# Kernel optimization log

Measured on AMD Instinct MI355X. Metric: run time of the kernel, lower is better.

The kernel has to match this reference:

```python
import jax, jax.numpy as jnp
import numpy as np

MULTI_INFER_NUM = 8
D_EMBED = 128
T, B = 512, 32


def setup_inputs() -> dict:
    key = jax.random.key(0)
    k1, k2, k3 = jax.random.split(key, 3)
    positions = jax.random.randint(k1, (T, B), 0, 16, dtype=jnp.int64)
    outputs = jax.random.normal(k2, (T, B, D_EMBED), dtype=jnp.float32)
    table = jax.random.normal(k3, (MULTI_INFER_NUM + 1, D_EMBED, D_EMBED), dtype=jnp.float32)
    return {"positions": positions, "outputs": outputs, "table": table}


def reference(positions, outputs, table):
    # clip positions >= multi_infer_num to the sentinel row multi_infer_num
    r_positions = jnp.where(positions < MULTI_INFER_NUM, positions, MULTI_INFER_NUM)
    # gather per-(t,b) d x d transfer matrices: [T, B, d, d]
    positions_embedding = table[r_positions]
    # batched matvec: [T, B, d]
    transferred = jnp.einsum('ibde,ibd->ibe', positions_embedding, outputs)
    return transferred
```

## Files before the change

kernel.cpp:

```cpp
#include <hip/hip_runtime.h>
#include <hip/hip_bf16.h>

#define TBPAIRS 16384
#define DEMB    128
#define NRROWS  9
#define BP      64

using short8 = __attribute__((ext_vector_type(8))) short;
using f32x4  = __attribute__((ext_vector_type(4))) float;

__device__ __forceinline__ unsigned short f2bf(float f) {
    unsigned u = __float_as_uint(f);
    u = u + 0x7FFFu + ((u >> 16) & 1u);
    return (unsigned short)(u >> 16);
}

__global__ __launch_bounds__(256) void pack_table_kernel(
    const float* __restrict__ table, uint4* __restrict__ bpack) {
    const int r = blockIdx.x;
    const float* M = table + r * DEMB * DEMB;
    for (int idx = threadIdx.x; idx < 2048; idx += 256) {
        const int lane = idx & 63;
        const int ks   = (idx >> 6) & 3;
        const int nt   = idx >> 8;
        const int e    = nt * 16 + (lane & 15);
        const int d0   = ks * 32 + (lane >> 4) * 8;
        union { unsigned short us[8]; uint4 v; } u;
#pragma unroll
        for (int j = 0; j < 8; ++j)
            u.us[j] = f2bf(M[(d0 + j) * DEMB + e]);
        bpack[r * 2048 + idx] = u.v;
    }
}

__global__ __launch_bounds__(256) void transfer_kernel(
    const int*   __restrict__ positions,
    const float* __restrict__ x,
    const uint4* __restrict__ bpack,
    float*       __restrict__ out) {

    __shared__ unsigned char list[NRROWS][BP];
    __shared__ int cnt[NRROWS];
    __shared__ unsigned char tile_r[16];
    __shared__ unsigned char tile_s[16];
    __shared__ int ntiles;

    const int tid   = threadIdx.x;
    const int pair0 = blockIdx.x * BP;

    if (tid < NRROWS) cnt[tid] = 0;
    __syncthreads();

    if (tid < BP) {
        int p = positions[pair0 + tid];
        int r = (p < 8) ? p : 8;
        int rank = atomicAdd(&cnt[r], 1);
        list[r][rank] = (unsigned char)tid;
    }
    __syncthreads();

    if (tid == 0) {
        int nt = 0;
        for (int r = 0; r < NRROWS; ++r)
            for (int s = 0; s < cnt[r]; s += 16) {
                tile_r[nt] = (unsigned char)r;
                tile_s[nt] = (unsigned char)s;
                ++nt;
            }
        ntiles = nt;
    }
    __syncthreads();

    const int wave = tid >> 6;
    const int lane = tid & 63;
    const int m16  = lane & 15;
    const int quad = lane >> 4;
    const int nt_total = ntiles;

    for (int t = wave; t < nt_total; t += 4) {
        const int r = tile_r[t];
        const int s = tile_s[t];
        const int c = cnt[r];

        const int slotA = (s + m16 < c) ? list[r][s + m16] : list[r][s];
        const float* xrow = x + (size_t)(pair0 + slotA) * DEMB;
        short8 a[4];
#pragma unroll
        for (int ks = 0; ks < 4; ++ks) {
            const float4* s4 = (const float4*)(xrow + ks * 32 + quad * 8);
            float4 f0 = s4[0];
            float4 f1 = s4[1];
            union { unsigned short us[8]; short8 s8; } ua;
            ua.us[0] = f2bf(f0.x); ua.us[1] = f2bf(f0.y);
            ua.us[2] = f2bf(f0.z); ua.us[3] = f2bf(f0.w);
            ua.us[4] = f2bf(f1.x); ua.us[5] = f2bf(f1.y);
            ua.us[6] = f2bf(f1.z); ua.us[7] = f2bf(f1.w);
            a[ks] = ua.s8;
        }

        int  prow[4];
        bool pval[4];
#pragma unroll
        for (int i = 0; i < 4; ++i) {
            const int m = quad * 4 + i;
            pval[i] = (s + m) < c;
            prow[i] = pval[i] ? (pair0 + list[r][s + m]) : 0;
        }

        const uint4* bp = bpack + r * 2048 + lane;
#pragma unroll
        for (int nt = 0; nt < 8; ++nt) {
            f32x4 acc = {0.f, 0.f, 0.f, 0.f};
#pragma unroll
            for (int ks = 0; ks < 4; ++ks) {
                union { uint4 v; short8 s8; } ub;
                ub.v = bp[(nt * 4 + ks) * 64];
                acc = __builtin_amdgcn_mfma_f32_16x16x32_bf16(a[ks], ub.s8, acc, 0, 0, 0);
            }
            const int col = nt * 16 + m16;
#pragma unroll
            for (int i = 0; i < 4; ++i)
                if (pval[i]) out[(size_t)prow[i] * DEMB + col] = acc[i];
        }
    }
}

extern "C" void kernel_launch(void* const* d_in, const int* in_sizes, int n_in,
                              void* d_out, int out_size, void* d_ws, size_t ws_size,
                              hipStream_t stream) {
    const int*   positions = (const int*)d_in[0];
    const float* outputs   = (const float*)d_in[1];
    const float* table     = (const float*)d_in[2];
    float* out = (float*)d_out;
    uint4* bpack = (uint4*)d_ws;

    hipLaunchKernelGGL(pack_table_kernel, dim3(NRROWS), dim3(256), 0, stream,
                       table, bpack);
    hipLaunchKernelGGL(transfer_kernel, dim3(TBPAIRS / BP), dim3(256), 0, stream,
                       positions, outputs, bpack, out);
}
```

Baseline: 82.68 us.

## Globally bucket pairs by table row before the MFMA transfer

Measured after the change: 80.74 us. -2.4%, faster.

```diff
diff --git a/kernel.cpp b/kernel.cpp
--- a/kernel.cpp
+++ b/kernel.cpp
@@ -3,8 +3,15 @@
 
 #define TBPAIRS 16384
 #define DEMB    128
-#define NRROWS  9
-#define BP      64
+#define NR      9
+#define CAP     16384
+#define CHUNK   64
+#define NCHUNK  (TBPAIRS / CHUNK)
+#define NVIRT   (NR * NCHUNK)
+#define GRID2   512
+
+#define BPACK_U4    (NR * 2048)
+#define BPACK_BYTES (BPACK_U4 * 16)
 
 using short8 = __attribute__((ext_vector_type(8))) short;
 using f32x4  = __attribute__((ext_vector_type(4))) float;
@@ -15,75 +22,78 @@
     return (unsigned short)(u >> 16);
 }
 
-__global__ __launch_bounds__(256) void pack_table_kernel(
-    const float* __restrict__ table, uint4* __restrict__ bpack) {
-    const int r = blockIdx.x;
-    const float* M = table + r * DEMB * DEMB;
-    for (int idx = threadIdx.x; idx < 2048; idx += 256) {
-        const int lane = idx & 63;
-        const int ks   = (idx >> 6) & 3;
-        const int nt   = idx >> 8;
-        const int e    = nt * 16 + (lane & 15);
-        const int d0   = ks * 32 + (lane >> 4) * 8;
-        union { unsigned short us[8]; uint4 v; } u;
+__global__ __launch_bounds__(256) void prep_kernel(
+    const int*   __restrict__ positions,
+    const float* __restrict__ table,
+    uint4* __restrict__ bpack,
+    int*   __restrict__ gcnt,
+    int*   __restrict__ perm) {
+
+    const int bid = blockIdx.x;
+    const int tid = threadIdx.x;
+
+    if (bid < 64) {
+        __shared__ int lcnt[NR];
+        __shared__ int lbase[NR];
+        if (tid < NR) lcnt[tid] = 0;
+        __syncthreads();
+        const int pair = bid * 256 + tid;
+        const int p = positions[pair];
+        const int r = (p < 8) ? p : 8;
+        const int rank = atomicAdd(&lcnt[r], 1);
+        __syncthreads();
+        if (tid < NR) lbase[tid] = atomicAdd(&gcnt[tid], lcnt[tid]);
+        __syncthreads();
+        perm[r * CAP + lbase[r] + rank] = pair;
+    } else {
+        const int pid = bid - 64;
+        const int r   = pid >> 2;
+        const int seg = pid & 3;
+        const float* M = table + r * DEMB * DEMB;
 #pragma unroll
-        for (int j = 0; j < 8; ++j)
-            u.us[j] = f2bf(M[(d0 + j) * DEMB + e]);
-        bpack[r * 2048 + idx] = u.v;
+        for (int k = 0; k < 2; ++k) {
+            const int idx  = seg * 512 + k * 256 + tid;
+            const int lane = idx & 63;
+            const int ks   = (idx >> 6) & 3;
+            const int nt   = idx >> 8;
+            const int e    = nt * 16 + (lane & 15);
+            const int d0   = ks * 32 + (lane >> 4) * 8;
+            union { unsigned short us[8]; uint4 v; } u;
+#pragma unroll
+            for (int j = 0; j < 8; ++j)
+                u.us[j] = f2bf(M[(d0 + j) * DEMB + e]);
+            bpack[r * 2048 + idx] = u.v;
+        }
     }
 }
 
 __global__ __launch_bounds__(256) void transfer_kernel(
-    const int*   __restrict__ positions,
     const float* __restrict__ x,
     const uint4* __restrict__ bpack,
+    const int*   __restrict__ gcnt,
+    const int*   __restrict__ perm,
     float*       __restrict__ out) {
 
-    __shared__ unsigned char list[NRROWS][BP];
-    __shared__ int cnt[NRROWS];
-    __shared__ unsigned char tile_r[16];
-    __shared__ unsigned char tile_s[16];
-    __shared__ int ntiles;
-
-    const int tid   = threadIdx.x;
-    const int pair0 = blockIdx.x * BP;
-
-    if (tid < NRROWS) cnt[tid] = 0;
-    __syncthreads();
-
-    if (tid < BP) {
-        int p = positions[pair0 + tid];
-        int r = (p < 8) ? p : 8;
-        int rank = atomicAdd(&cnt[r], 1);
-        list[r][rank] = (unsigned char)tid;
-    }
-    __syncthreads();
-
-    if (tid == 0) {
-        int nt = 0;
-        for (int r = 0; r < NRROWS; ++r)
-            for (int s = 0; s < cnt[r]; s += 16) {
-                tile_r[nt] = (unsigned char)r;
-                tile_s[nt] = (unsigned char)s;
-                ++nt;
-            }
-        ntiles = nt;
-    }
-    __syncthreads();
-
+    const int tid  = threadIdx.x;
     const int wave = tid >> 6;
     const int lane = tid & 63;
     const int m16  = lane & 15;
     const int quad = lane >> 4;
-    const int nt_total = ntiles;
 
-    for (int t = wave; t < nt_total; t += 4) {
-        const int r = tile_r[t];
-        const int s = tile_s[t];
-        const int c = cnt[r];
+    for (int v = blockIdx.x; v < NVIRT; v += GRID2) {
+        const int r     = v % NR;
+        const int chunk = v / NR;
+        const int c     = gcnt[r];
+        const int base  = chunk * CHUNK;
+        if (base >= c) continue;
+        const int tb = base + wave * 16;
+        if (tb >= c) continue;
+        const int nm = c - tb;
 
-        const int slotA = (s + m16 < c) ? list[r][s + m16] : list[r][s];
-        const float* xrow = x + (size_t)(pair0 + slotA) * DEMB;
+        const int* pr = perm + r * CAP + tb;
+
+        const int slotA = pr[(m16 < nm) ? m16 : 0];
+        const float* xrow = x + (size_t)slotA * DEMB;
         short8 a[4];
 #pragma unroll
         for (int ks = 0; ks < 4; ++ks) {
@@ -103,18 +113,18 @@
 #pragma unroll
         for (int i = 0; i < 4; ++i) {
             const int m = quad * 4 + i;
-            pval[i] = (s + m) < c;
-            prow[i] = pval[i] ? (pair0 + list[r][s + m]) : 0;
+            pval[i] = m < nm;
+            prow[i] = pval[i] ? pr[m] : 0;
         }
 
         const uint4* bp = bpack + r * 2048 + lane;
-#pragma unroll
+#pragma unroll 2
         for (int nt = 0; nt < 8; ++nt) {
             f32x4 acc = {0.f, 0.f, 0.f, 0.f};
 #pragma unroll
             for (int ks = 0; ks < 4; ++ks) {
-                union { uint4 v; short8 s8; } ub;
-                ub.v = bp[(nt * 4 + ks) * 64];
+                union { uint4 v4; short8 s8; } ub;
+                ub.v4 = bp[(nt * 4 + ks) * 64];
                 acc = __builtin_amdgcn_mfma_f32_16x16x32_bf16(a[ks], ub.s8, acc, 0, 0, 0);
             }
             const int col = nt * 16 + m16;
@@ -132,10 +142,15 @@
     const float* outputs   = (const float*)d_in[1];
     const float* table     = (const float*)d_in[2];
     float* out = (float*)d_out;
+
     uint4* bpack = (uint4*)d_ws;
+    int*   gcnt  = (int*)((char*)d_ws + BPACK_BYTES);
+    int*   perm  = (int*)((char*)d_ws + BPACK_BYTES + 64);
 
-    hipLaunchKernelGGL(pack_table_kernel, dim3(NRROWS), dim3(256), 0, stream,
-                       table, bpack);
-    hipLaunchKernelGGL(transfer_kernel, dim3(TBPAIRS / BP), dim3(256), 0, stream,
-                       positions, outputs, bpack, out);
+    hipMemsetAsync((void*)gcnt, 0, 64, stream);
+
+    hipLaunchKernelGGL(prep_kernel, dim3(100), dim3(256), 0, stream,
+                       positions, table, bpack, gcnt, perm);
+    hipLaunchKernelGGL(transfer_kernel, dim3(GRID2), dim3(256), 0, stream,
+                       outputs, bpack, gcnt, perm, out);
 }
```
